# Optimization experiments

Measured on AMD Instinct MI355X. Metric: run time of the kernel, lower is better.

The kernel has to match this reference:

```python
import jax, jax.numpy as jnp
import numpy as np

B, S, DIM, H, DH = 1, 4096, 2048, 16, 128
EPS = 1e-5


def setup_inputs() -> dict:
    key = jax.random.key(0)
    ks = jax.random.split(key, 16)
    sc = 0.02
    inp = {
        'hidden_states': jax.random.normal(ks[0], (B, S, DIM), jnp.float32),
        'freqs_cos': jax.random.uniform(ks[1], (1, S, 1, DH), jnp.float32),
        'freqs_sin': jax.random.uniform(ks[2], (1, S, 1, DH), jnp.float32),
        'Wq': jax.random.normal(ks[3], (DIM, DIM), jnp.float32) * sc,
        'bq': jax.random.normal(ks[4], (DIM,), jnp.float32) * sc,
        'Wk': jax.random.normal(ks[5], (DIM, DIM), jnp.float32) * sc,
        'bk': jax.random.normal(ks[6], (DIM,), jnp.float32) * sc,
        'Wv': jax.random.normal(ks[7], (DIM, DIM), jnp.float32) * sc,
        'bv': jax.random.normal(ks[8], (DIM,), jnp.float32) * sc,
        'Wo': jax.random.normal(ks[9], (DIM, DIM), jnp.float32) * sc,
        'bo': jax.random.normal(ks[10], (DIM,), jnp.float32) * sc,
        'gq': jnp.ones((DIM,), jnp.float32),
        'gk': jnp.ones((DIM,), jnp.float32),
    }
    return inp


def _rmsnorm(x, g):
    var = jnp.mean(jnp.square(x), axis=-1, keepdims=True)
    return x * jax.lax.rsqrt(var + EPS) * g


def _apply_rope(x, freqs_cos, freqs_sin):
    # x: [B,S,H,DH]; interleaved rotary as in WanAttnProcessor
    x1 = x[..., 0::2]
    x2 = x[..., 1::2]
    cos = freqs_cos[..., 0::2]
    sin = freqs_sin[..., 1::2]
    o1 = x1 * cos - x2 * sin
    o2 = x1 * sin + x2 * cos
    return jnp.stack([o1, o2], axis=-1).reshape(x.shape)


def reference(hidden_states, freqs_cos, freqs_sin, Wq, bq, Wk, bk, Wv, bv, Wo, bo, gq, gk):
    q = hidden_states @ Wq + bq
    k = hidden_states @ Wk + bk
    v = hidden_states @ Wv + bv
    q = _rmsnorm(q, gq)
    k = _rmsnorm(k, gk)
    q = q.reshape(B, S, H, DH)
    k = k.reshape(B, S, H, DH)
    v = v.reshape(B, S, H, DH)
    q = _apply_rope(q, freqs_cos, freqs_sin)
    k = _apply_rope(k, freqs_cos, freqs_sin)
    scale = 1.0 / np.sqrt(DH).astype(np.float32)
    scores = jnp.einsum('bqhd,bkhd->bhqk', q, k) * scale
    attn = jax.nn.softmax(scores, axis=-1)
    out = jnp.einsum('bhqk,bkhd->bqhd', attn, v)
    out = out.reshape(B, S, H * DH)
    return out @ Wo + bo
```

## Files before the change

### kernel.cpp

```cpp
#include <hip/hip_runtime.h>
#include <hip/hip_bf16.h>

#define SEQ 4096
#define DIMC 2048
#define NH 16
#define DHD 128

typedef short s8v __attribute__((ext_vector_type(8)));
typedef float f4v __attribute__((ext_vector_type(4)));
typedef __bf16 bf8 __attribute__((ext_vector_type(8)));
typedef float f4 __attribute__((ext_vector_type(4)));
typedef float f16v __attribute__((ext_vector_type(16)));
typedef int i4v __attribute__((ext_vector_type(4)));

typedef __attribute__((address_space(3))) void lds_t;
typedef __attribute__((address_space(1))) void gbl_t;

__device__ __attribute__((aligned(256))) short g_h[(size_t)SEQ * DIMC];
__device__ __attribute__((aligned(256))) short g_q[(size_t)SEQ * DIMC];
__device__ __attribute__((aligned(256))) short g_k[(size_t)SEQ * DIMC];
__device__ __attribute__((aligned(256))) short g_v[(size_t)SEQ * DIMC];
__device__ __attribute__((aligned(256))) short g_vt[(size_t)DIMC * SEQ];
__device__ __attribute__((aligned(256))) short g_wt[4][(size_t)DIMC * DIMC];

__device__ __forceinline__ float b2f(short s) {
    union { unsigned u; float f; } v;
    v.u = ((unsigned)(unsigned short)s) << 16;
    return v.f;
}
__device__ __forceinline__ short f2b(float f) {
    union { float f; unsigned u; } v;
    v.f = f;
    unsigned b = v.u;
    b += 0x7FFFu + ((b >> 16) & 1u);
    return (short)(b >> 16);
}
__device__ __forceinline__ f4 mfma16(bf8 a, bf8 b, f4 c) {
    return __builtin_amdgcn_mfma_f32_16x16x32_bf16(a, b, c, 0, 0, 0);
}
__device__ __forceinline__ f16v mfma32(bf8 a, bf8 b, f16v c) {
    return __builtin_amdgcn_mfma_f32_32x32x16_bf16(a, b, c, 0, 0, 0);
}
__device__ __forceinline__ void gl_lds16(const short* g, short* l) {
    __builtin_amdgcn_global_load_lds((gbl_t*)g, (lds_t*)l, 16, 0, 0);
}
__device__ __forceinline__ void plane32_swap(int& a, int& b) {
    asm volatile("v_permlane32_swap_b32 %0, %1" : "+v"(a), "+v"(b));
}
__device__ __forceinline__ int pk2b(float a, float b) {
    int r;
    asm("v_cvt_pk_bf16_f32 %0, %1, %2" : "=v"(r) : "v"(a), "v"(b));
    return r;
}

__global__ __launch_bounds__(256) void conv_h(const float* __restrict__ src) {
    size_t i = ((size_t)blockIdx.x * 256 + threadIdx.x) * 8;
    f4v u0 = *reinterpret_cast<const f4v*>(src + i);
    f4v u1 = *reinterpret_cast<const f4v*>(src + i + 4);
    s8v t;
    for (int j = 0; j < 4; ++j) { t[j] = f2b(u0[j]); t[4 + j] = f2b(u1[j]); }
    *reinterpret_cast<s8v*>(g_h + i) = t;
}

__global__ __launch_bounds__(256) void prep_w(const float* __restrict__ W0,
                                              const float* __restrict__ W1,
                                              const float* __restrict__ W2,
                                              const float* __restrict__ W3) {
    __shared__ __attribute__((aligned(16))) float t[64][68];
    const int z = blockIdx.z;
    const float* W = (z == 0) ? W0 : (z == 1) ? W1 : (z == 2) ? W2 : W3;
    short* WT = g_wt[z];
    const int r0 = blockIdx.y * 64, c0 = blockIdx.x * 64;
    const int tid = threadIdx.x;
    for (int i = 0; i < 4; ++i) {
        int slot = tid + i * 256;
        int r = slot >> 4, c4 = (slot & 15) * 4;
        *reinterpret_cast<f4v*>(&t[r][c4]) =
            *reinterpret_cast<const f4v*>(&W[(size_t)(r0 + r) * DIMC + c0 + c4]);
    }
    __syncthreads();
    for (int i = 0; i < 2; ++i) {
        int slot = tid + i * 256;
        int n = slot >> 3, k8 = (slot & 7) * 8;
        s8v o;
        for (int j = 0; j < 8; ++j) o[j] = f2b(t[k8 + j][n]);
        *reinterpret_cast<s8v*>(&WT[(size_t)(c0 + n) * DIMC + r0 + k8]) = o;
    }
}

template <int DSTF>
__device__ __forceinline__ void gemm_body(const short* __restrict__ X,
                                          const short* __restrict__ Bw,
                                          const float* __restrict__ bias,
                                          short* __restrict__ Yb,
                                          float* __restrict__ Yf,
                                          int bm, int bn) {
    __shared__ __attribute__((aligned(16))) short As[128 * 32];
    __shared__ __attribute__((aligned(16))) short Bs[128 * 32];
    const int tid = threadIdx.x;
    const int w = tid >> 6, lane = tid & 63;
    const int l16 = lane & 15, quad = lane >> 4;
    const int wm = w & 1, wn = w >> 1;

    f4 acc[4][4];
    for (int mi = 0; mi < 4; ++mi)
        for (int ni = 0; ni < 4; ++ni) acc[mi][ni] = (f4)0.0f;

    const int s0 = tid, s1 = tid + 256;
    const int ra0 = s0 >> 2, ca0 = (s0 & 3) * 8;
    const int ra1 = s1 >> 2, ca1 = (s1 & 3) * 8;
    const size_t xo0 = (size_t)(bm * 128 + ra0) * DIMC + ca0;
    const size_t xo1 = (size_t)(bm * 128 + ra1) * DIMC + ca1;
    const size_t bo0 = (size_t)(bn * 128 + ra0) * DIMC + ca0;
    const size_t bo1 = (size_t)(bn * 128 + ra1) * DIMC + ca1;
    short* lda0 = As + (size_t)(0 * 256 + w * 64) * 8;
    short* lda1 = As + (size_t)(1 * 256 + w * 64) * 8;
    short* ldb0 = Bs + (size_t)(0 * 256 + w * 64) * 8;
    short* ldb1 = Bs + (size_t)(1 * 256 + w * 64) * 8;

    for (int kb = 0; kb < DIMC; kb += 32) {
        __syncthreads();
        gl_lds16(X + xo0 + kb, lda0);
        gl_lds16(X + xo1 + kb, lda1);
        gl_lds16(Bw + bo0 + kb, ldb0);
        gl_lds16(Bw + bo1 + kb, ldb1);
        __syncthreads();
        bf8 af[4], bfr[4];
        for (int mi = 0; mi < 4; ++mi)
            af[mi] = *reinterpret_cast<const bf8*>(As + (wm * 64 + mi * 16 + l16) * 32 + quad * 8);
        for (int ni = 0; ni < 4; ++ni)
            bfr[ni] = *reinterpret_cast<const bf8*>(Bs + (wn * 64 + ni * 16 + l16) * 32 + quad * 8);
        for (int mi = 0; mi < 4; ++mi)
            for (int ni = 0; ni < 4; ++ni)
                acc[mi][ni] = mfma16(af[mi], bfr[ni], acc[mi][ni]);
    }

    for (int ni = 0; ni < 4; ++ni) {
        int col = bn * 128 + wn * 64 + ni * 16 + l16;
        float bcol = bias[col];
        for (int mi = 0; mi < 4; ++mi) {
            int row = bm * 128 + wm * 64 + mi * 16 + quad * 4;
            for (int r = 0; r < 4; ++r) {
                if (DSTF)
                    Yf[(size_t)(row + r) * DIMC + col] = acc[mi][ni][r] + bcol;
                else
                    Yb[(size_t)(row + r) * DIMC + col] = f2b(acc[mi][ni][r] + bcol);
            }
        }
    }
}

__global__ __launch_bounds__(256, 2) void gemm_qkv(const float* __restrict__ bq,
                                                   const float* __restrict__ bk,
                                                   const float* __restrict__ bv) {
    const int z = blockIdx.z;
    const float* bias = (z == 0) ? bq : (z == 1) ? bk : bv;
    short* Y = (z == 0) ? g_q : (z == 1) ? g_k : g_v;
    gemm_body<0>(g_h, g_wt[z], bias, Y, nullptr, blockIdx.y, blockIdx.x);
}

__global__ __launch_bounds__(256, 2) void gemm_o(const float* __restrict__ bias,
                                                 float* __restrict__ Yf) {
    gemm_body<1>(g_q, g_wt[3], bias, nullptr, Yf, blockIdx.y, blockIdx.x);
}

__global__ __launch_bounds__(256) void rmsnorm_rope(const float* __restrict__ gq,
                                                    const float* __restrict__ gk,
                                                    const float* __restrict__ fc,
                                                    const float* __restrict__ fs) {
    __shared__ float partial[4];
    __shared__ float totsh;
    const int s = blockIdx.x;
    const int which = blockIdx.y;
    short* x = which ? g_k : g_q;
    const float* g = which ? gk : gq;
    const int tid = threadIdx.x;
    const int d0 = tid * 8;

    s8v xv = *reinterpret_cast<const s8v*>(&x[(size_t)s * DIMC + d0]);
    float xf[8];
    float ssq = 0.0f;
    for (int j = 0; j < 8; ++j) { xf[j] = b2f(xv[j]); ssq += xf[j] * xf[j]; }
    for (int off = 32; off; off >>= 1) ssq += __shfl_down(ssq, off);
    if ((tid & 63) == 0) partial[tid >> 6] = ssq;
    __syncthreads();
    if (tid == 0) totsh = partial[0] + partial[1] + partial[2] + partial[3];
    __syncthreads();
    float rs = rsqrtf(totsh * (1.0f / (float)DIMC) + 1e-5f);
    if (which == 0) rs *= 0.12751744f;

    f4v g0 = *reinterpret_cast<const f4v*>(&g[d0]);
    f4v g1 = *reinterpret_cast<const f4v*>(&g[d0 + 4]);
    float xn[8];
    for (int j = 0; j < 4; ++j) { xn[j] = xf[j] * rs * g0[j]; xn[4 + j] = xf[4 + j] * rs * g1[j]; }

    s8v ov;
    for (int p = 0; p < 4; ++p) {
        int e = d0 + 2 * p;
        int hd = e & (DHD - 1);
        float c = fc[(size_t)s * DHD + hd];
        float sn = fs[(size_t)s * DHD + hd + 1];
        float x1 = xn[2 * p], x2 = xn[2 * p + 1];
        ov[2 * p]     = f2b(x1 * c - x2 * sn);
        ov[2 * p + 1] = f2b(x1 * sn + x2 * c);
    }
    *reinterpret_cast<s8v*>(&x[(size_t)s * DIMC + d0]) = ov;
}

__global__ __launch_bounds__(256) void transpose_v() {
    __shared__ __attribute__((aligned(16))) short t[64][72];
    const int h = blockIdx.z, dt = blockIdx.y, st = blockIdx.x;
    const int tid = threadIdx.x;
    const short* src = g_v + (size_t)st * 64 * DIMC + h * DHD + dt * 64;
    for (int i = 0; i < 2; ++i) {
        int slot = tid + i * 256;
        int s = slot >> 3, d8 = (slot & 7) * 8;
        *reinterpret_cast<s8v*>(&t[s][d8]) =
            *reinterpret_cast<const s8v*>(src + (size_t)s * DIMC + d8);
    }
    __syncthreads();
    short* dst = g_vt + (size_t)(h * DHD + dt * 64) * SEQ + st * 64;
    for (int i = 0; i < 2; ++i) {
        int slot = tid + i * 256;
        int d = slot >> 3, s8_ = (slot & 7) * 8;
        s8v o;
        for (int j = 0; j < 8; ++j) o[j] = t[s8_ + j][d];
        *reinterpret_cast<s8v*>(dst + (size_t)d * SEQ + s8_) = o;
    }
}

__global__ __launch_bounds__(256, 2) void attn_k() {
    __shared__ __attribute__((aligned(16))) short Ks0[2][64 * 128];
    __shared__ __attribute__((aligned(16))) short Vt0[2][128 * 64];

    const int h = blockIdx.y;
    const int q0 = blockIdx.x * 128;
    const int tid = threadIdx.x;
    const int w = tid >> 6, lane = tid & 63;
    const int l32 = lane & 31, hf = lane >> 5;
    const int l16 = lane & 15;
    const int cbase = hf + l16;
    const int khl = hf + l32;

    bf8 qf[8];
    {
        const short* qb = g_q + (size_t)(q0 + w * 32 + l32) * DIMC + h * DHD + hf * 8;
#pragma unroll
        for (int dc = 0; dc < 8; ++dc)
            qf[dc] = *reinterpret_cast<const bf8*>(qb + dc * 16);
    }

    f16v of[4];
#pragma unroll
    for (int i = 0; i < 4; ++i) of[i] = (f16v)0.0f;
    f16v lacc = (f16v)0.0f;
    const f16v fz = (f16v)0.0f;

    s8v ob;
#pragma unroll
    for (int j = 0; j < 8; ++j) ob[j] = (short)0x3F80;
    const bf8 vones = __builtin_bit_cast(bf8, ob);

    const short* Kbase = g_k + h * DHD;
    const short* Vbase = g_vt + (size_t)h * DHD * SEQ;

    const short* kp[4];
    const short* vp[4];
#pragma unroll
    for (int i = 0; i < 4; ++i) {
        int s = tid + i * 256;
        int krow = s >> 4, kcb = ((s & 15) - krow) & 15;
        int vd = s >> 3, vkb = ((s & 7) - vd) & 7;
        kp[i] = Kbase + (size_t)krow * DIMC + kcb * 8;
        vp[i] = Vbase + (size_t)vd * SEQ + vkb * 8;
    }

#pragma unroll
    for (int i = 0; i < 4; ++i) {
        gl_lds16(kp[i], &Ks0[0][(size_t)(i * 256 + w * 64) * 8]);
        kp[i] += (size_t)64 * DIMC;
    }
#pragma unroll
    for (int i = 0; i < 4; ++i) {
        gl_lds16(vp[i], &Vt0[0][(size_t)(i * 256 + w * 64) * 8]);
        vp[i] += 64;
    }

    for (int kt = 0; kt < SEQ; kt += 64) {
        const int cur = (kt >> 6) & 1;
        if (kt + 64 < SEQ) {
            const int nxt = cur ^ 1;
#pragma unroll
            for (int i = 0; i < 4; ++i) {
                gl_lds16(kp[i], &Ks0[nxt][(size_t)(i * 256 + w * 64) * 8]);
                kp[i] += (size_t)64 * DIMC;
            }
#pragma unroll
            for (int i = 0; i < 4; ++i) {
                gl_lds16(vp[i], &Vt0[nxt][(size_t)(i * 256 + w * 64) * 8]);
                vp[i] += 64;
            }
            asm volatile("s_waitcnt vmcnt(8)" ::: "memory");
        } else {
            asm volatile("s_waitcnt vmcnt(0)" ::: "memory");
        }
        __builtin_amdgcn_sched_barrier(0);
        __builtin_amdgcn_s_barrier();
        __builtin_amdgcn_sched_barrier(0);

        const short* Ks = Ks0[cur];
        const short* Vt = Vt0[cur];

#pragma unroll
        for (int kc = 0; kc < 2; ++kc) {
            const short* krb = Ks + (kc * 32 + l32) * 128;
            __builtin_amdgcn_s_setprio(1);
            f16v sa = mfma32(*reinterpret_cast<const bf8*>(krb + ((cbase & 15) << 3)), qf[0], fz);
#pragma unroll
            for (int dc = 1; dc < 8; ++dc) {
                bf8 kf = *reinterpret_cast<const bf8*>(krb + (((dc * 2 + cbase) & 15) << 3));
                sa = mfma32(kf, qf[dc], sa);
            }
            __builtin_amdgcn_s_setprio(0);

            int wv[8];
#pragma unroll
            for (int t = 0; t < 8; ++t) {
                float e0 = exp2f(sa[2 * t]);
                float e1 = exp2f(sa[2 * t + 1]);
                wv[t] = pk2b(e0, e1);
            }
            int a0 = wv[0], b0 = wv[2]; plane32_swap(a0, b0);
            int a1 = wv[1], b1 = wv[3]; plane32_swap(a1, b1);
            int a2 = wv[4], b2 = wv[6]; plane32_swap(a2, b2);
            int a3 = wv[5], b3 = wv[7]; plane32_swap(a3, b3);
            i4v pw0 = {a0, a1, b0, b1};
            i4v pw1 = {a2, a3, b2, b3};
            bf8 pa0 = __builtin_bit_cast(bf8, pw0);
            bf8 pa1 = __builtin_bit_cast(bf8, pw1);

            __builtin_amdgcn_s_setprio(1);
            lacc = mfma32(pa0, vones, lacc);
            lacc = mfma32(pa1, vones, lacc);

#pragma unroll
            for (int kp2 = 0; kp2 < 2; ++kp2) {
                bf8 pa = kp2 ? pa1 : pa0;
#pragma unroll
                for (int dcb = 0; dcb < 4; ++dcb) {
                    int d = dcb * 32 + l32;
                    int ks = (kc * 4 + kp2 * 2 + khl) & 7;
                    bf8 vf = *reinterpret_cast<const bf8*>(Vt + d * 64 + ks * 8);
                    of[dcb] = mfma32(pa, vf, of[dcb]);
                }
            }
            __builtin_amdgcn_s_setprio(0);
        }

        __builtin_amdgcn_s_barrier();
        __builtin_amdgcn_sched_barrier(0);
    }

#pragma unroll
    for (int r = 0; r < 16; ++r) {
        float iv = 1.0f / lacc[r];
        int row = q0 + w * 32 + (r & 3) + 8 * (r >> 2) + 4 * hf;
#pragma unroll
        for (int dcb = 0; dcb < 4; ++dcb)
            g_q[(size_t)row * DIMC + h * DHD + dcb * 32 + l32] = f2b(of[dcb][r] * iv);
    }
}

extern "C" void kernel_launch(void* const* d_in, const int* in_sizes, int n_in,
                              void* d_out, int out_size, void* d_ws, size_t ws_size,
                              hipStream_t stream) {
    const float* hidden = (const float*)d_in[0];
    const float* fc = (const float*)d_in[1];
    const float* fs = (const float*)d_in[2];
    const float* Wq = (const float*)d_in[3];
    const float* bq = (const float*)d_in[4];
    const float* Wk = (const float*)d_in[5];
    const float* bk = (const float*)d_in[6];
    const float* Wv = (const float*)d_in[7];
    const float* bv = (const float*)d_in[8];
    const float* Wo = (const float*)d_in[9];
    const float* bo = (const float*)d_in[10];
    const float* gq = (const float*)d_in[11];
    const float* gk = (const float*)d_in[12];

    dim3 blk(256);
    conv_h<<<dim3(4096), blk, 0, stream>>>(hidden);
    prep_w<<<dim3(32, 32, 4), blk, 0, stream>>>(Wq, Wk, Wv, Wo);
    gemm_qkv<<<dim3(16, 32, 3), blk, 0, stream>>>(bq, bk, bv);
    rmsnorm_rope<<<dim3(SEQ, 2), blk, 0, stream>>>(gq, gk, fc, fs);
    transpose_v<<<dim3(64, 2, NH), blk, 0, stream>>>();
    attn_k<<<dim3(32, NH), blk, 0, stream>>>();
    gemm_o<<<dim3(16, 32), blk, 0, stream>>>(bo, (float*)d_out);
}
```

Baseline: 538.6 us.

## Split attention key tile across two wave groups and reduce partials in LDS

The attention block grows from 4 to 8 waves. Each pair of waves shares the same 32 query rows but handles a different 32-key half of every 64-key tile, so one pass replaces the old two-chunk inner loop. At the end, the second group writes its partial output and row-sum accumulators into the reused K/V shared memory, and the first group adds them in and writes the normalized result. The aim is more waves per CU to hide MFMA and LDS latency and a shorter dependency chain per wave. The cost is a cross-wave reduction with extra barriers, and occupancy may be limited by registers under the new 512-thread launch bound.

```diff
diff --git a/kernel.cpp b/kernel.cpp
--- a/kernel.cpp
+++ b/kernel.cpp
@@ -229,7 +229,7 @@
     }
 }
 
-__global__ __launch_bounds__(256, 2) void attn_k() {
+__global__ __launch_bounds__(512, 4) void attn_k() {
     __shared__ __attribute__((aligned(16))) short Ks0[2][64 * 128];
     __shared__ __attribute__((aligned(16))) short Vt0[2][128 * 64];
 
@@ -237,6 +237,7 @@
     const int q0 = blockIdx.x * 128;
     const int tid = threadIdx.x;
     const int w = tid >> 6, lane = tid & 63;
+    const int wq = w & 3, wk = w >> 2;
     const int l32 = lane & 31, hf = lane >> 5;
     const int l16 = lane & 15;
     const int cbase = hf + l16;
@@ -244,7 +245,7 @@
 
     bf8 qf[8];
     {
-        const short* qb = g_q + (size_t)(q0 + w * 32 + l32) * DIMC + h * DHD + hf * 8;
+        const short* qb = g_q + (size_t)(q0 + wq * 32 + l32) * DIMC + h * DHD + hf * 8;
 #pragma unroll
         for (int dc = 0; dc < 8; ++dc)
             qf[dc] = *reinterpret_cast<const bf8*>(qb + dc * 16);
@@ -264,11 +265,11 @@
     const short* Kbase = g_k + h * DHD;
     const short* Vbase = g_vt + (size_t)h * DHD * SEQ;
 
-    const short* kp[4];
-    const short* vp[4];
-#pragma unroll
-    for (int i = 0; i < 4; ++i) {
-        int s = tid + i * 256;
+    const short* kp[2];
+    const short* vp[2];
+#pragma unroll
+    for (int i = 0; i < 2; ++i) {
+        int s = tid + i * 512;
         int krow = s >> 4, kcb = ((s & 15) - krow) & 15;
         int vd = s >> 3, vkb = ((s & 7) - vd) & 7;
         kp[i] = Kbase + (size_t)krow * DIMC + kcb * 8;
@@ -276,13 +277,13 @@
     }
 
 #pragma unroll
-    for (int i = 0; i < 4; ++i) {
-        gl_lds16(kp[i], &Ks0[0][(size_t)(i * 256 + w * 64) * 8]);
+    for (int i = 0; i < 2; ++i) {
+        gl_lds16(kp[i], &Ks0[0][(size_t)(i * 512 + w * 64) * 8]);
         kp[i] += (size_t)64 * DIMC;
     }
 #pragma unroll
-    for (int i = 0; i < 4; ++i) {
-        gl_lds16(vp[i], &Vt0[0][(size_t)(i * 256 + w * 64) * 8]);
+    for (int i = 0; i < 2; ++i) {
+        gl_lds16(vp[i], &Vt0[0][(size_t)(i * 512 + w * 64) * 8]);
         vp[i] += 64;
     }
 
@@ -291,16 +292,16 @@
         if (kt + 64 < SEQ) {
             const int nxt = cur ^ 1;
 #pragma unroll
-            for (int i = 0; i < 4; ++i) {
-                gl_lds16(kp[i], &Ks0[nxt][(size_t)(i * 256 + w * 64) * 8]);
+            for (int i = 0; i < 2; ++i) {
+                gl_lds16(kp[i], &Ks0[nxt][(size_t)(i * 512 + w * 64) * 8]);
                 kp[i] += (size_t)64 * DIMC;
             }
 #pragma unroll
-            for (int i = 0; i < 4; ++i) {
-                gl_lds16(vp[i], &Vt0[nxt][(size_t)(i * 256 + w * 64) * 8]);
+            for (int i = 0; i < 2; ++i) {
+                gl_lds16(vp[i], &Vt0[nxt][(size_t)(i * 512 + w * 64) * 8]);
                 vp[i] += 64;
             }
-            asm volatile("s_waitcnt vmcnt(8)" ::: "memory");
+            asm volatile("s_waitcnt vmcnt(4)" ::: "memory");
         } else {
             asm volatile("s_waitcnt vmcnt(0)" ::: "memory");
         }
@@ -311,63 +312,95 @@
         const short* Ks = Ks0[cur];
         const short* Vt = Vt0[cur];
 
-#pragma unroll
-        for (int kc = 0; kc < 2; ++kc) {
-            const short* krb = Ks + (kc * 32 + l32) * 128;
-            __builtin_amdgcn_s_setprio(1);
-            f16v sa = mfma32(*reinterpret_cast<const bf8*>(krb + ((cbase & 15) << 3)), qf[0], fz);
-#pragma unroll
-            for (int dc = 1; dc < 8; ++dc) {
-                bf8 kf = *reinterpret_cast<const bf8*>(krb + (((dc * 2 + cbase) & 15) << 3));
-                sa = mfma32(kf, qf[dc], sa);
+        const short* krb = Ks + (wk * 32 + l32) * 128;
+        __builtin_amdgcn_s_setprio(1);
+        f16v sa = mfma32(*reinterpret_cast<const bf8*>(krb + ((cbase & 15) << 3)), qf[0], fz);
+#pragma unroll
+        for (int dc = 1; dc < 8; ++dc) {
+            bf8 kf = *reinterpret_cast<const bf8*>(krb + (((dc * 2 + cbase) & 15) << 3));
+            sa = mfma32(kf, qf[dc], sa);
+        }
+        __builtin_amdgcn_s_setprio(0);
+
+        int wv[8];
+#pragma unroll
+        for (int t = 0; t < 8; ++t) {
+            float e0 = exp2f(sa[2 * t]);
+            float e1 = exp2f(sa[2 * t + 1]);
+            wv[t] = pk2b(e0, e1);
+        }
+        int a0 = wv[0], b0 = wv[2]; plane32_swap(a0, b0);
+        int a1 = wv[1], b1 = wv[3]; plane32_swap(a1, b1);
+        int a2 = wv[4], b2 = wv[6]; plane32_swap(a2, b2);
+        int a3 = wv[5], b3 = wv[7]; plane32_swap(a3, b3);
+        i4v pw0 = {a0, a1, b0, b1};
+        i4v pw1 = {a2, a3, b2, b3};
+        bf8 pa0 = __builtin_bit_cast(bf8, pw0);
+        bf8 pa1 = __builtin_bit_cast(bf8, pw1);
+
+        __builtin_amdgcn_s_setprio(1);
+        lacc = mfma32(pa0, vones, lacc);
+        lacc = mfma32(pa1, vones, lacc);
+
+#pragma unroll
+        for (int kp2 = 0; kp2 < 2; ++kp2) {
+            bf8 pa = kp2 ? pa1 : pa0;
+#pragma unroll
+            for (int dcb = 0; dcb < 4; ++dcb) {
+                int d = dcb * 32 + l32;
+                int ks = (wk * 4 + kp2 * 2 + khl) & 7;
+                bf8 vf = *reinterpret_cast<const bf8*>(Vt + d * 64 + ks * 8);
+                of[dcb] = mfma32(pa, vf, of[dcb]);
             }
-            __builtin_amdgcn_s_setprio(0);
-
-            int wv[8];
-#pragma unroll
-            for (int t = 0; t < 8; ++t) {
-                float e0 = exp2f(sa[2 * t]);
-                float e1 = exp2f(sa[2 * t + 1]);
-                wv[t] = pk2b(e0, e1);
-            }
-            int a0 = wv[0], b0 = wv[2]; plane32_swap(a0, b0);
-            int a1 = wv[1], b1 = wv[3]; plane32_swap(a1, b1);
-            int a2 = wv[4], b2 = wv[6]; plane32_swap(a2, b2);
-            int a3 = wv[5], b3 = wv[7]; plane32_swap(a3, b3);
-            i4v pw0 = {a0, a1, b0, b1};
-            i4v pw1 = {a2, a3, b2, b3};
-            bf8 pa0 = __builtin_bit_cast(bf8, pw0);
-            bf8 pa1 = __builtin_bit_cast(bf8, pw1);
-
-            __builtin_amdgcn_s_setprio(1);
-            lacc = mfma32(pa0, vones, lacc);
-            lacc = mfma32(pa1, vones, lacc);
-
-#pragma unroll
-            for (int kp2 = 0; kp2 < 2; ++kp2) {
-                bf8 pa = kp2 ? pa1 : pa0;
-#pragma unroll
-                for (int dcb = 0; dcb < 4; ++dcb) {
-                    int d = dcb * 32 + l32;
-                    int ks = (kc * 4 + kp2 * 2 + khl) & 7;
-                    bf8 vf = *reinterpret_cast<const bf8*>(Vt + d * 64 + ks * 8);
-                    of[dcb] = mfma32(pa, vf, of[dcb]);
-                }
-            }
-            __builtin_amdgcn_s_setprio(0);
-        }
+        }
+        __builtin_amdgcn_s_setprio(0);
 
         __builtin_amdgcn_s_barrier();
         __builtin_amdgcn_sched_barrier(0);
     }
 
-#pragma unroll
-    for (int r = 0; r < 16; ++r) {
-        float iv = 1.0f / lacc[r];
-        int row = q0 + w * 32 + (r & 3) + 8 * (r >> 2) + 4 * hf;
-#pragma unroll
-        for (int dcb = 0; dcb < 4; ++dcb)
-            g_q[(size_t)row * DIMC + h * DHD + dcb * 32 + l32] = f2b(of[dcb][r] * iv);
+    __syncthreads();
+    float* pO = (float*)(&Ks0[0][0]);
+    float* pL = (float*)(&Vt0[0][0]);
+    if (wk == 1) {
+#pragma unroll
+        for (int r = 0; r < 16; ++r)
+            pL[(wq * 16 + r) * 64 + lane] = lacc[r];
+    }
+#pragma unroll
+    for (int halfd = 0; halfd < 2; ++halfd) {
+        if (wk == 1) {
+#pragma unroll
+            for (int d2 = 0; d2 < 2; ++d2)
+#pragma unroll
+                for (int r = 0; r < 16; ++r)
+                    pO[((wq * 2 + d2) * 16 + r) * 64 + lane] = of[halfd * 2 + d2][r];
+        }
+        __syncthreads();
+        if (wk == 0) {
+#pragma unroll
+            for (int d2 = 0; d2 < 2; ++d2)
+#pragma unroll
+                for (int r = 0; r < 16; ++r)
+                    of[halfd * 2 + d2][r] += pO[((wq * 2 + d2) * 16 + r) * 64 + lane];
+            if (halfd == 0) {
+#pragma unroll
+                for (int r = 0; r < 16; ++r)
+                    lacc[r] += pL[(wq * 16 + r) * 64 + lane];
+            }
+        }
+        __syncthreads();
+    }
+
+    if (wk == 0) {
+#pragma unroll
+        for (int r = 0; r < 16; ++r) {
+            float iv = 1.0f / lacc[r];
+            int row = q0 + wq * 32 + (r & 3) + 8 * (r >> 2) + 4 * hf;
+#pragma unroll
+            for (int dcb = 0; dcb < 4; ++dcb)
+                g_q[(size_t)row * DIMC + h * DHD + dcb * 32 + l32] = f2b(of[dcb][r] * iv);
+        }
     }
 }
 
@@ -394,6 +427,6 @@
     gemm_qkv<<<dim3(16, 32, 3), blk, 0, stream>>>(bq, bk, bv);
     rmsnorm_rope<<<dim3(SEQ, 2), blk, 0, stream>>>(gq, gk, fc, fs);
     transpose_v<<<dim3(64, 2, NH), blk, 0, stream>>>();
-    attn_k<<<dim3(32, NH), blk, 0, stream>>>();
+    attn_k<<<dim3(32, NH), dim3(512), 0, stream>>>();
     gemm_o<<<dim3(16, 32), blk, 0, stream>>>(bo, (float*)d_out);
 }
```

Result: slower. 721.2 us (+33.9%).
